# Kernel tuning notes

Measured on AMD Instinct MI355X. Metric: run time of the kernel, lower is better.

## Reference

```python
import jax, jax.numpy as jnp
import numpy as np

EPS = 1e-5
FT_DEPTH = 5
FT_SMOOTH = 1e-5


def _conv(x, w):
    # x: [B,H,W,Cin], w: [kh,kw,Cin,Cout], SAME padding, stride 1
    return jax.lax.conv_general_dilated(x, w, (1, 1), 'SAME',
                                         dimension_numbers=('NHWC', 'HWIO', 'NHWC'))


def _bn(x, g, b, m, v):
    # inference-mode batch norm over last axis
    return (x - m) * jax.lax.rsqrt(v + EPS) * g + b


def _ftanimoto(p, l, axis):
    # Fractal Tanimoto similarity with keepdims, averaged over FT_DEPTH scales.
    tpl = jnp.sum(p * l, axis=axis, keepdims=True)
    tpp = jnp.sum(p * p, axis=axis, keepdims=True)
    tll = jnp.sum(l * l, axis=axis, keepdims=True)
    num = tpl + FT_SMOOTH
    denum = jnp.zeros_like(tpl)
    for d in range(FT_DEPTH):
        a = 2.0 ** d
        b = -(2.0 * a - 1.0)
        denum = denum + 1.0 / (a * (tpp + tll) + b * tpl + FT_SMOOTH)
    return num * denum * (1.0 / FT_DEPTH)


def setup_inputs() -> dict:
    key = jax.random.key(0)
    ks = jax.random.split(key, 24)
    B, H, W, C = 8, 128, 128, 96
    d = {}
    d['x1'] = jax.random.normal(ks[0], (B, H, W, C), jnp.float32)
    d['x2'] = jax.random.normal(ks[1], (B, H, W, C), jnp.float32)
    d['x3'] = jax.random.normal(ks[2], (B, H, W, C), jnp.float32)
    d['wq'] = jax.random.normal(ks[3], (3, 3, C, C), jnp.float32) * 0.05
    d['gq'] = jax.random.uniform(ks[4], (C,), jnp.float32)
    d['bq'] = jax.random.normal(ks[5], (C,), jnp.float32) * 0.1
    d['mq'] = jax.random.normal(ks[6], (C,), jnp.float32) * 0.1
    d['vq'] = jax.random.uniform(ks[7], (C,), jnp.float32) + 0.5
    d['wk'] = jax.random.normal(ks[8], (3, 3, C, C), jnp.float32) * 0.05
    d['gk'] = jax.random.uniform(ks[9], (C,), jnp.float32)
    d['bk'] = jax.random.normal(ks[10], (C,), jnp.float32) * 0.1
    d['mk'] = jax.random.normal(ks[11], (C,), jnp.float32) * 0.1
    d['vk'] = jax.random.uniform(ks[12], (C,), jnp.float32) + 0.5
    d['wv'] = jax.random.normal(ks[13], (3, 3, C, C), jnp.float32) * 0.05
    d['gv'] = jax.random.uniform(ks[14], (C,), jnp.float32)
    d['bv'] = jax.random.normal(ks[15], (C,), jnp.float32) * 0.1
    d['mv'] = jax.random.normal(ks[16], (C,), jnp.float32) * 0.1
    d['vv'] = jax.random.uniform(ks[17], (C,), jnp.float32) + 0.5
    d['gn'] = jax.random.uniform(ks[18], (C,), jnp.float32)
    d['bnb'] = jax.random.normal(ks[19], (C,), jnp.float32) * 0.1
    d['mn'] = jax.random.normal(ks[20], (C,), jnp.float32) * 0.1
    d['vn'] = jax.random.uniform(ks[21], (C,), jnp.float32) + 0.5
    return d


def reference(x1, x2, x3, wq, gq, bq, mq, vq, wk, gk, bk, mk, vk,
              wv, gv, bv, mv, vv, gn, bnb, mn, vn):
    q = jax.nn.sigmoid(_bn(_conv(x1, wq), gq, bq, mq, vq))   # [B,H,W,C]
    k = jax.nn.sigmoid(_bn(_conv(x2, wk), gk, bk, mk, vk))
    v = jax.nn.sigmoid(_bn(_conv(x3, wv), gv, bv, mv, vv))
    att_spat = _ftanimoto(q, k, axis=-1)        # [B,H,W,1] spatial attention
    att_chan = _ftanimoto(q, k, axis=(1, 2))    # [B,1,1,C] channel attention
    v_cspat = 0.5 * (att_chan * v + att_spat * v)
    return _bn(v_cspat, gn, bnb, mn, vn)
```

## Files before the change

### kernel.cpp

```cpp
#include <hip/hip_runtime.h>
#include <hip/hip_bf16.h>
#include <math.h>

#define BB 8
#define HH 128
#define WW 128
#define CC 96
#define NPIX (BB*HH*WW)
#define EPSF 1e-5f
#define FT_SMOOTH_F 1e-5f
#define ROWB 8320
#define WELEM 82944

typedef short short8 __attribute__((ext_vector_type(8)));
typedef float f32x4 __attribute__((ext_vector_type(4)));

__device__ __forceinline__ float ftanimoto(float tpl, float tpp, float tll) {
    float num = tpl + FT_SMOOTH_F;
    float denum = 0.0f;
    float a = 1.0f;
#pragma unroll
    for (int d = 0; d < 5; ++d) {
        float bco = -(2.0f * a - 1.0f);
        denum += 1.0f / (a * (tpp + tll) + bco * tpl + FT_SMOOTH_F);
        a *= 2.0f;
    }
    return num * denum * 0.2f;
}

__device__ __forceinline__ unsigned short f2bf(float f) {
    __hip_bfloat16 h = __float2bfloat16(f);
    return *(unsigned short*)&h;
}

__device__ __forceinline__ float bf2f(unsigned short u) {
    return __uint_as_float((unsigned int)u << 16);
}

__global__ __launch_bounds__(256) void cast_wT2(
    const float* __restrict__ wq, const float* __restrict__ wk,
    const float* __restrict__ wv, unsigned short* __restrict__ wT2)
{
    const int tid = blockIdx.x * 256 + threadIdx.x;
    if (tid >= 3 * WELEM) return;
    const int cid = tid / WELEM;
    const int o = tid - cid * WELEM;
    const int j = o & 7;
    const int rest = o >> 3;
    const int lq = rest & 63;
    const int lrow = lq >> 2, qq = lq & 3;
    const int tile = rest >> 6;
    const int nt = tile % 6;
    const int tcc = tile / 6;
    const int cc = tcc % 3, tap = tcc / 3;
    const int ci = cc * 32 + qq * 8 + j;
    const int co = nt * 16 + lrow;
    const float* w = (cid == 0) ? wq : (cid == 1) ? wk : wv;
    wT2[tid] = f2bf(w[(size_t)(tap * CC + ci) * CC + co]);
}

__global__ __launch_bounds__(256, 3) void conv_all(
    const float* __restrict__ x1, const float* __restrict__ x2,
    const float* __restrict__ x3, const unsigned short* __restrict__ wT2,
    const float* __restrict__ gq, const float* __restrict__ bq,
    const float* __restrict__ mq, const float* __restrict__ vq,
    const float* __restrict__ gk, const float* __restrict__ bk,
    const float* __restrict__ mk, const float* __restrict__ vk,
    const float* __restrict__ gv, const float* __restrict__ bv,
    const float* __restrict__ mv, const float* __restrict__ vv,
    unsigned short* __restrict__ qb, unsigned short* __restrict__ kb,
    unsigned short* __restrict__ vb)
{
    __shared__ __align__(16) char smem[4 * ROWB];
    const int tid = threadIdx.x;
    const int wv = tid >> 6;
    const int L  = tid & 63;
    const int cid = blockIdx.x >> 9;
    const int blk = blockIdx.x & 511;
    const int b  = blk >> 6;
    const int h0 = (blk & 63) << 1;
    const int hrow = h0 + (wv >> 1);
    const int wwbase = (wv & 1) << 6;
    const int lrow = L & 15;
    const int qq = L >> 4;

    const float* xsrc = (cid == 0) ? x1 : (cid == 1) ? x2 : x3;
    const unsigned short* wT2p = wT2 + (size_t)cid * WELEM;

    const int hst = h0 - 1 + wv;
    const bool stv = (hst >= 0) && (hst < HH);
    const float* xrow = xsrc + (size_t)(b * HH + (stv ? hst : 0)) * WW * CC;
    char* myrow = smem + wv * ROWB;

    f32x4 acc[4][6];
#pragma unroll
    for (int mt = 0; mt < 4; ++mt)
#pragma unroll
        for (int nt = 0; nt < 6; ++nt) acc[mt][nt] = (f32x4){0.f, 0.f, 0.f, 0.f};

    for (int cc = 0; cc < 3; ++cc) {
        __syncthreads();
        if (stv) {
#pragma unroll
            for (int it = 0; it < 9; ++it) {
                const int idx = it * 64 + L;
                if (idx < 520) {
                    const int p = idx >> 2;
                    const int c = idx & 3;
                    const int w = p - 1;
                    short8 o = (short8){0,0,0,0,0,0,0,0};
                    if (w >= 0 && w < WW) {
                        const float* src = xrow + (size_t)w * CC + cc * 32 + c * 8;
                        const float4 a0 = *(const float4*)src;
                        const float4 a1 = *(const float4*)(src + 4);
                        o[0] = (short)f2bf(a0.x); o[1] = (short)f2bf(a0.y);
                        o[2] = (short)f2bf(a0.z); o[3] = (short)f2bf(a0.w);
                        o[4] = (short)f2bf(a1.x); o[5] = (short)f2bf(a1.y);
                        o[6] = (short)f2bf(a1.z); o[7] = (short)f2bf(a1.w);
                    }
                    const int slot = c ^ ((p ^ (p >> 2)) & 3);
                    *(short8*)(myrow + p * 64 + slot * 16) = o;
                }
            }
        }
        __syncthreads();
#pragma unroll
        for (int dy = -1; dy <= 1; ++dy) {
            const int hh = hrow + dy;
            if (hh < 0 || hh >= HH) continue;
            const char* ldsrow = smem + (dy + 1 + (wv >> 1)) * ROWB;
#pragma unroll
            for (int dx = -1; dx <= 1; ++dx) {
                const int tap = (dy + 1) * 3 + (dx + 1);
                const unsigned short* bsrc = wT2p + (size_t)(tap * 3 + cc) * 6 * 512;
                short8 bf[6];
#pragma unroll
                for (int nt = 0; nt < 6; ++nt)
                    bf[nt] = *(const short8*)(bsrc + nt * 512 + (lrow * 4 + qq) * 8);
                short8 af[4];
#pragma unroll
                for (int mt = 0; mt < 4; ++mt) {
                    const int p = wwbase + mt * 16 + lrow + dx + 1;
                    const int slot = qq ^ ((p ^ (p >> 2)) & 3);
                    af[mt] = *(const short8*)(ldsrow + p * 64 + slot * 16);
                }
#pragma unroll
                for (int nt = 0; nt < 6; ++nt)
#pragma unroll
                    for (int mt = 0; mt < 4; ++mt)
                        acc[mt][nt] = __builtin_amdgcn_mfma_f32_16x16x32_bf16(
                            af[mt], bf[nt], acc[mt][nt], 0, 0, 0);
            }
        }
    }

    const float* g  = (cid == 0) ? gq : (cid == 1) ? gk : gv;
    const float* bt = (cid == 0) ? bq : (cid == 1) ? bk : bv;
    const float* mu = (cid == 0) ? mq : (cid == 1) ? mk : mv;
    const float* var = (cid == 0) ? vq : (cid == 1) ? vk : vv;
    unsigned short* outp = (cid == 0) ? qb : (cid == 1) ? kb : vb;

#pragma unroll
    for (int nt = 0; nt < 6; ++nt) {
        const int co = nt * 16 + lrow;
        const float scl = g[co] * rsqrtf(var[co] + EPSF);
        const float sft = bt[co] - mu[co] * scl;
#pragma unroll
        for (int mt = 0; mt < 4; ++mt) {
#pragma unroll
            for (int r = 0; r < 4; ++r) {
                const int row = (wv << 6) + (mt << 4) + (qq << 2) + r;
                const int h = h0 + (row >> 7);
                const int w = row & 127;
                const size_t pix = (size_t)(b * HH + h) * WW + w;
                const float t = acc[mt][nt][r] * scl + sft;
                outp[pix * CC + co] = f2bf(1.0f / (1.0f + expf(-t)));
            }
        }
    }
}

__global__ __launch_bounds__(256) void spatial_att(
    const unsigned short* __restrict__ qb, const unsigned short* __restrict__ kb,
    float* __restrict__ atts)
{
    const int gid = blockIdx.x * 256 + threadIdx.x;
    const int pix = gid >> 6;
    const int lane = threadIdx.x & 63;
    float tpl = 0.f, tpp = 0.f, tll = 0.f;
    if (lane < 48) {
        const unsigned int qu = ((const unsigned int*)qb)[(size_t)pix * 48 + lane];
        const unsigned int ku = ((const unsigned int*)kb)[(size_t)pix * 48 + lane];
        const float q0 = __uint_as_float(qu << 16);
        const float q1 = __uint_as_float(qu & 0xffff0000u);
        const float k0 = __uint_as_float(ku << 16);
        const float k1 = __uint_as_float(ku & 0xffff0000u);
        tpl = q0 * k0 + q1 * k1;
        tpp = q0 * q0 + q1 * q1;
        tll = k0 * k0 + k1 * k1;
    }
#pragma unroll
    for (int off = 32; off > 0; off >>= 1) {
        tpl += __shfl_xor(tpl, off);
        tpp += __shfl_xor(tpp, off);
        tll += __shfl_xor(tll, off);
    }
    if (lane == 0) atts[pix] = ftanimoto(tpl, tpp, tll);
}

__global__ __launch_bounds__(192) void chan_partial(
    const unsigned short* __restrict__ qb, const unsigned short* __restrict__ kb,
    float* __restrict__ part)
{
    __shared__ float red[16][12][24];
    const int t = threadIdx.x;
    const int g = t / 12;
    const int c8 = t - g * 12;
    const int b = blockIdx.x >> 6;
    const int slab = blockIdx.x & 63;
    const size_t p0 = (size_t)b * HH * WW + (size_t)slab * 256;

    float s_tpl[8], s_tpp[8], s_tll[8];
#pragma unroll
    for (int j = 0; j < 8; ++j) { s_tpl[j] = 0.f; s_tpp[j] = 0.f; s_tll[j] = 0.f; }

    for (int i = 0; i < 16; ++i) {
        const size_t pe = (p0 + g + i * 16) * CC + c8 * 8;
        const short8 qv = *(const short8*)(qb + pe);
        const short8 kv = *(const short8*)(kb + pe);
#pragma unroll
        for (int j = 0; j < 8; ++j) {
            const float qf = bf2f((unsigned short)qv[j]);
            const float kf = bf2f((unsigned short)kv[j]);
            s_tpl[j] = fmaf(qf, kf, s_tpl[j]);
            s_tpp[j] = fmaf(qf, qf, s_tpp[j]);
            s_tll[j] = fmaf(kf, kf, s_tll[j]);
        }
    }
#pragma unroll
    for (int j = 0; j < 8; ++j) {
        red[g][c8][0 * 8 + j] = s_tpl[j];
        red[g][c8][1 * 8 + j] = s_tpp[j];
        red[g][c8][2 * 8 + j] = s_tll[j];
    }
    __syncthreads();
    if (t < CC) {
        const int cg = t >> 3, cj = t & 7;
        float tpl = 0.f, tpp = 0.f, tll = 0.f;
        for (int gg = 0; gg < 16; ++gg) {
            tpl += red[gg][cg][0 * 8 + cj];
            tpp += red[gg][cg][1 * 8 + cj];
            tll += red[gg][cg][2 * 8 + cj];
        }
        const size_t idx = ((size_t)blockIdx.x * CC + t) * 3;
        part[idx + 0] = tpl;
        part[idx + 1] = tpp;
        part[idx + 2] = tll;
    }
}

__global__ __launch_bounds__(128) void chan_final(
    const float* __restrict__ part, float* __restrict__ attc)
{
    const int b = blockIdx.x;
    const int c = threadIdx.x;
    if (c >= CC) return;
    float tpl = 0.f, tpp = 0.f, tll = 0.f;
    for (int s = 0; s < 64; ++s) {
        const size_t idx = (((size_t)(b * 64 + s)) * CC + c) * 3;
        tpl += part[idx + 0];
        tpp += part[idx + 1];
        tll += part[idx + 2];
    }
    attc[b * CC + c] = ftanimoto(tpl, tpp, tll);
}

__global__ __launch_bounds__(256) void final_combine(
    const unsigned short* __restrict__ vb, const float* __restrict__ atts,
    const float* __restrict__ attc,
    const float* __restrict__ gn, const float* __restrict__ bnb,
    const float* __restrict__ mn, const float* __restrict__ vn,
    float* __restrict__ out)
{
    const int tid = blockIdx.x * 256 + threadIdx.x;
    const int c8 = tid % 12;
    const int pix = tid / 12;
    const int b = pix >> 14;
    const short8 v = *(const short8*)(vb + (size_t)pix * CC + c8 * 8);
    const float as = atts[pix];
    float r[8];
#pragma unroll
    for (int j = 0; j < 8; ++j) {
        const int co = c8 * 8 + j;
        const float nscl = gn[co] * rsqrtf(vn[co] + EPSF);
        const float nsft = bnb[co] - mn[co] * nscl;
        const float att = 0.5f * (attc[b * CC + co] + as);
        r[j] = att * bf2f((unsigned short)v[j]) * nscl + nsft;
    }
    float* dst = out + (size_t)pix * CC + c8 * 8;
    *(float4*)dst = make_float4(r[0], r[1], r[2], r[3]);
    *(float4*)(dst + 4) = make_float4(r[4], r[5], r[6], r[7]);
}

extern "C" void kernel_launch(void* const* d_in, const int* in_sizes, int n_in,
                              void* d_out, int out_size, void* d_ws, size_t ws_size,
                              hipStream_t stream)
{
    const float* x1 = (const float*)d_in[0];
    const float* x2 = (const float*)d_in[1];
    const float* x3 = (const float*)d_in[2];
    const float* wq = (const float*)d_in[3];
    const float* gq = (const float*)d_in[4];
    const float* bq = (const float*)d_in[5];
    const float* mq = (const float*)d_in[6];
    const float* vq = (const float*)d_in[7];
    const float* wk = (const float*)d_in[8];
    const float* gk = (const float*)d_in[9];
    const float* bk = (const float*)d_in[10];
    const float* mk = (const float*)d_in[11];
    const float* vk = (const float*)d_in[12];
    const float* wvw = (const float*)d_in[13];
    const float* gv = (const float*)d_in[14];
    const float* bv = (const float*)d_in[15];
    const float* mv = (const float*)d_in[16];
    const float* vv = (const float*)d_in[17];
    const float* gn = (const float*)d_in[18];
    const float* bnb = (const float*)d_in[19];
    const float* mn = (const float*)d_in[20];
    const float* vn = (const float*)d_in[21];

    unsigned short* wT2 = (unsigned short*)d_ws;
    unsigned short* vb = wT2 + (size_t)3 * WELEM;
    float* atts = (float*)(vb + (size_t)NPIX * CC);
    float* part = atts + NPIX;
    float* attc = part + (size_t)512 * CC * 3;

    unsigned short* qb = (unsigned short*)d_out;
    unsigned short* kb = qb + (size_t)NPIX * CC;

    cast_wT2<<<(3 * WELEM + 255) / 256, 256, 0, stream>>>(wq, wk, wvw, wT2);
    conv_all<<<1536, 256, 0, stream>>>(x1, x2, x3, wT2,
                                       gq, bq, mq, vq, gk, bk, mk, vk,
                                       gv, bv, mv, vv, qb, kb, vb);
    spatial_att<<<NPIX / 4, 256, 0, stream>>>(qb, kb, atts);
    chan_partial<<<BB * 64, 192, 0, stream>>>(qb, kb, part);
    chan_final<<<BB, 128, 0, stream>>>(part, attc);
    final_combine<<<NPIX * 12 / 256, 256, 0, stream>>>(vb, atts, attc,
                                                       gn, bnb, mn, vn,
                                                       (float*)d_out);
}
```

Before: 366.5 us.

## Prefetch conv input into registers and fuse spatial and channel attention reductions

The conv kernel now loads the next channel chunk of input rows into registers while MFMA runs on the current chunk, so global load latency overlaps with compute. The occupancy hint drops from 3 to 2 blocks to make room for the extra registers. The separate spatial-attention and channel-partial kernels are merged into one pass that reads q and k once and produces both per-pixel and per-channel sums via shared memory. The channel final reduction becomes a wave-per-channel shuffle reduction. This adds register pressure and shared memory use in exchange for less global traffic and fewer launches.

```diff
diff --git a/kernel.cpp b/kernel.cpp
--- a/kernel.cpp
+++ b/kernel.cpp
@@ -59,7 +59,7 @@
     wT2[tid] = f2bf(w[(size_t)(tap * CC + ci) * CC + co]);
 }
 
-__global__ __launch_bounds__(256, 3) void conv_all(
+__global__ __launch_bounds__(256, 2) void conv_all(
     const float* __restrict__ x1, const float* __restrict__ x2,
     const float* __restrict__ x3, const unsigned short* __restrict__ wT2,
     const float* __restrict__ gq, const float* __restrict__ bq,
@@ -73,24 +73,24 @@
 {
     __shared__ __align__(16) char smem[4 * ROWB];
     const int tid = threadIdx.x;
-    const int wv = tid >> 6;
+    const int wvi = tid >> 6;
     const int L  = tid & 63;
     const int cid = blockIdx.x >> 9;
     const int blk = blockIdx.x & 511;
     const int b  = blk >> 6;
     const int h0 = (blk & 63) << 1;
-    const int hrow = h0 + (wv >> 1);
-    const int wwbase = (wv & 1) << 6;
+    const int hrow = h0 + (wvi >> 1);
+    const int wwbase = (wvi & 1) << 6;
     const int lrow = L & 15;
     const int qq = L >> 4;
 
     const float* xsrc = (cid == 0) ? x1 : (cid == 1) ? x2 : x3;
     const unsigned short* wT2p = wT2 + (size_t)cid * WELEM;
 
-    const int hst = h0 - 1 + wv;
+    const int hst = h0 - 1 + wvi;
     const bool stv = (hst >= 0) && (hst < HH);
     const float* xrow = xsrc + (size_t)(b * HH + (stv ? hst : 0)) * WW * CC;
-    char* myrow = smem + wv * ROWB;
+    char* myrow = smem + wvi * ROWB;
 
     f32x4 acc[4][6];
 #pragma unroll
@@ -98,61 +98,85 @@
 #pragma unroll
         for (int nt = 0; nt < 6; ++nt) acc[mt][nt] = (f32x4){0.f, 0.f, 0.f, 0.f};
 
-    for (int cc = 0; cc < 3; ++cc) {
-        __syncthreads();
-        if (stv) {
-#pragma unroll
-            for (int it = 0; it < 9; ++it) {
-                const int idx = it * 64 + L;
-                if (idx < 520) {
-                    const int p = idx >> 2;
-                    const int c = idx & 3;
-                    const int w = p - 1;
-                    short8 o = (short8){0,0,0,0,0,0,0,0};
-                    if (w >= 0 && w < WW) {
-                        const float* src = xrow + (size_t)w * CC + cc * 32 + c * 8;
-                        const float4 a0 = *(const float4*)src;
-                        const float4 a1 = *(const float4*)(src + 4);
-                        o[0] = (short)f2bf(a0.x); o[1] = (short)f2bf(a0.y);
-                        o[2] = (short)f2bf(a0.z); o[3] = (short)f2bf(a0.w);
-                        o[4] = (short)f2bf(a1.x); o[5] = (short)f2bf(a1.y);
-                        o[6] = (short)f2bf(a1.z); o[7] = (short)f2bf(a1.w);
-                    }
-                    const int slot = c ^ ((p ^ (p >> 2)) & 3);
-                    *(short8*)(myrow + p * 64 + slot * 16) = o;
-                }
-            }
-        }
-        __syncthreads();
-#pragma unroll
-        for (int dy = -1; dy <= 1; ++dy) {
-            const int hh = hrow + dy;
-            if (hh < 0 || hh >= HH) continue;
-            const char* ldsrow = smem + (dy + 1 + (wv >> 1)) * ROWB;
-#pragma unroll
-            for (int dx = -1; dx <= 1; ++dx) {
-                const int tap = (dy + 1) * 3 + (dx + 1);
-                const unsigned short* bsrc = wT2p + (size_t)(tap * 3 + cc) * 6 * 512;
-                short8 bf[6];
-#pragma unroll
-                for (int nt = 0; nt < 6; ++nt)
-                    bf[nt] = *(const short8*)(bsrc + nt * 512 + (lrow * 4 + qq) * 8);
-                short8 af[4];
-#pragma unroll
-                for (int mt = 0; mt < 4; ++mt) {
-                    const int p = wwbase + mt * 16 + lrow + dx + 1;
-                    const int slot = qq ^ ((p ^ (p >> 2)) & 3);
-                    af[mt] = *(const short8*)(ldsrow + p * 64 + slot * 16);
-                }
-#pragma unroll
-                for (int nt = 0; nt < 6; ++nt)
-#pragma unroll
-                    for (int mt = 0; mt < 4; ++mt)
-                        acc[mt][nt] = __builtin_amdgcn_mfma_f32_16x16x32_bf16(
-                            af[mt], bf[nt], acc[mt][nt], 0, 0, 0);
-            }
-        }
-    }
+    float4 pre[9][2];
+
+#define PREF(ccv) do { if (stv) { _Pragma("unroll") \
+    for (int it = 0; it < 9; ++it) { \
+        const int idx = it * 64 + L; \
+        if (idx < 520) { \
+            const int p = idx >> 2; \
+            const int c = idx & 3; \
+            const int w = p - 1; \
+            if (w >= 0 && w < WW) { \
+                const float* src = xrow + (size_t)w * CC + (ccv) * 32 + c * 8; \
+                pre[it][0] = *(const float4*)src; \
+                pre[it][1] = *(const float4*)(src + 4); \
+            } } } } } while (0)
+
+#define WST() do { if (stv) { _Pragma("unroll") \
+    for (int it = 0; it < 9; ++it) { \
+        const int idx = it * 64 + L; \
+        if (idx < 520) { \
+            const int p = idx >> 2; \
+            const int c = idx & 3; \
+            const int w = p - 1; \
+            short8 o = (short8){0,0,0,0,0,0,0,0}; \
+            if (w >= 0 && w < WW) { \
+                o[0] = (short)f2bf(pre[it][0].x); o[1] = (short)f2bf(pre[it][0].y); \
+                o[2] = (short)f2bf(pre[it][0].z); o[3] = (short)f2bf(pre[it][0].w); \
+                o[4] = (short)f2bf(pre[it][1].x); o[5] = (short)f2bf(pre[it][1].y); \
+                o[6] = (short)f2bf(pre[it][1].z); o[7] = (short)f2bf(pre[it][1].w); \
+            } \
+            const int slot = c ^ ((p ^ (p >> 2)) & 3); \
+            *(short8*)(myrow + p * 64 + slot * 16) = o; \
+        } } } } while (0)
+
+#define COMPUTE(ccv) do { _Pragma("unroll") \
+    for (int dy = -1; dy <= 1; ++dy) { \
+        const int hh = hrow + dy; \
+        if (hh < 0 || hh >= HH) continue; \
+        const char* ldsrow = smem + (dy + 1 + (wvi >> 1)) * ROWB; \
+        _Pragma("unroll") \
+        for (int dx = -1; dx <= 1; ++dx) { \
+            const int tap = (dy + 1) * 3 + (dx + 1); \
+            const unsigned short* bsrc = wT2p + (size_t)(tap * 3 + (ccv)) * 6 * 512; \
+            short8 bfr[6]; \
+            _Pragma("unroll") \
+            for (int nt = 0; nt < 6; ++nt) \
+                bfr[nt] = *(const short8*)(bsrc + nt * 512 + (lrow * 4 + qq) * 8); \
+            short8 afr[4]; \
+            _Pragma("unroll") \
+            for (int mt = 0; mt < 4; ++mt) { \
+                const int p = wwbase + mt * 16 + lrow + dx + 1; \
+                const int slot = qq ^ ((p ^ (p >> 2)) & 3); \
+                afr[mt] = *(const short8*)(ldsrow + p * 64 + slot * 16); \
+            } \
+            _Pragma("unroll") \
+            for (int nt = 0; nt < 6; ++nt) \
+                _Pragma("unroll") \
+                for (int mt = 0; mt < 4; ++mt) \
+                    acc[mt][nt] = __builtin_amdgcn_mfma_f32_16x16x32_bf16( \
+                        afr[mt], bfr[nt], acc[mt][nt], 0, 0, 0); \
+        } } } while (0)
+
+    PREF(0);
+    WST();
+    __syncthreads();
+    PREF(1);
+    COMPUTE(0);
+    __syncthreads();
+    WST();
+    __syncthreads();
+    PREF(2);
+    COMPUTE(1);
+    __syncthreads();
+    WST();
+    __syncthreads();
+    COMPUTE(2);
+
+#undef PREF
+#undef WST
+#undef COMPUTE
 
     const float* g  = (cid == 0) ? gq : (cid == 1) ? gk : gv;
     const float* bt = (cid == 0) ? bq : (cid == 1) ? bk : bv;
@@ -169,7 +193,7 @@
         for (int mt = 0; mt < 4; ++mt) {
 #pragma unroll
             for (int r = 0; r < 4; ++r) {
-                const int row = (wv << 6) + (mt << 4) + (qq << 2) + r;
+                const int row = (wvi << 6) + (mt << 4) + (qq << 2) + r;
                 const int h = h0 + (row >> 7);
                 const int w = row & 127;
                 const size_t pix = (size_t)(b * HH + h) * WW + w;
@@ -180,54 +204,28 @@
     }
 }
 
-__global__ __launch_bounds__(256) void spatial_att(
+__global__ __launch_bounds__(192) void qk_att(
     const unsigned short* __restrict__ qb, const unsigned short* __restrict__ kb,
-    float* __restrict__ atts)
-{
-    const int gid = blockIdx.x * 256 + threadIdx.x;
-    const int pix = gid >> 6;
-    const int lane = threadIdx.x & 63;
-    float tpl = 0.f, tpp = 0.f, tll = 0.f;
-    if (lane < 48) {
-        const unsigned int qu = ((const unsigned int*)qb)[(size_t)pix * 48 + lane];
-        const unsigned int ku = ((const unsigned int*)kb)[(size_t)pix * 48 + lane];
-        const float q0 = __uint_as_float(qu << 16);
-        const float q1 = __uint_as_float(qu & 0xffff0000u);
-        const float k0 = __uint_as_float(ku << 16);
-        const float k1 = __uint_as_float(ku & 0xffff0000u);
-        tpl = q0 * k0 + q1 * k1;
-        tpp = q0 * q0 + q1 * q1;
-        tll = k0 * k0 + k1 * k1;
-    }
-#pragma unroll
-    for (int off = 32; off > 0; off >>= 1) {
-        tpl += __shfl_xor(tpl, off);
-        tpp += __shfl_xor(tpp, off);
-        tll += __shfl_xor(tll, off);
-    }
-    if (lane == 0) atts[pix] = ftanimoto(tpl, tpp, tll);
-}
-
-__global__ __launch_bounds__(192) void chan_partial(
-    const unsigned short* __restrict__ qb, const unsigned short* __restrict__ kb,
-    float* __restrict__ part)
-{
+    float* __restrict__ atts, float* __restrict__ part)
+{
+    __shared__ float pxr[256][37];
     __shared__ float red[16][12][24];
     const int t = threadIdx.x;
     const int g = t / 12;
     const int c8 = t - g * 12;
-    const int b = blockIdx.x >> 6;
-    const int slab = blockIdx.x & 63;
-    const size_t p0 = (size_t)b * HH * WW + (size_t)slab * 256;
+    const size_t p0 = (size_t)blockIdx.x * 256;
 
     float s_tpl[8], s_tpp[8], s_tll[8];
 #pragma unroll
     for (int j = 0; j < 8; ++j) { s_tpl[j] = 0.f; s_tpp[j] = 0.f; s_tll[j] = 0.f; }
 
+#pragma unroll
     for (int i = 0; i < 16; ++i) {
-        const size_t pe = (p0 + g + i * 16) * CC + c8 * 8;
+        const int px = g + i * 16;
+        const size_t pe = (p0 + px) * CC + c8 * 8;
         const short8 qv = *(const short8*)(qb + pe);
         const short8 kv = *(const short8*)(kb + pe);
+        float ptpl = 0.f, ptpp = 0.f, ptll = 0.f;
 #pragma unroll
         for (int j = 0; j < 8; ++j) {
             const float qf = bf2f((unsigned short)qv[j]);
@@ -235,22 +233,40 @@
             s_tpl[j] = fmaf(qf, kf, s_tpl[j]);
             s_tpp[j] = fmaf(qf, qf, s_tpp[j]);
             s_tll[j] = fmaf(kf, kf, s_tll[j]);
+            ptpl = fmaf(qf, kf, ptpl);
+            ptpp = fmaf(qf, qf, ptpp);
+            ptll = fmaf(kf, kf, ptll);
         }
+        pxr[px][c8 * 3 + 0] = ptpl;
+        pxr[px][c8 * 3 + 1] = ptpp;
+        pxr[px][c8 * 3 + 2] = ptll;
     }
 #pragma unroll
     for (int j = 0; j < 8; ++j) {
-        red[g][c8][0 * 8 + j] = s_tpl[j];
-        red[g][c8][1 * 8 + j] = s_tpp[j];
-        red[g][c8][2 * 8 + j] = s_tll[j];
-    }
-    __syncthreads();
+        red[g][c8][j]      = s_tpl[j];
+        red[g][c8][8 + j]  = s_tpp[j];
+        red[g][c8][16 + j] = s_tll[j];
+    }
+    __syncthreads();
+
+    for (int px = t; px < 256; px += 192) {
+        float tpl = 0.f, tpp = 0.f, tll = 0.f;
+#pragma unroll
+        for (int c = 0; c < 12; ++c) {
+            tpl += pxr[px][c * 3 + 0];
+            tpp += pxr[px][c * 3 + 1];
+            tll += pxr[px][c * 3 + 2];
+        }
+        atts[p0 + px] = ftanimoto(tpl, tpp, tll);
+    }
+
     if (t < CC) {
         const int cg = t >> 3, cj = t & 7;
         float tpl = 0.f, tpp = 0.f, tll = 0.f;
         for (int gg = 0; gg < 16; ++gg) {
-            tpl += red[gg][cg][0 * 8 + cj];
-            tpp += red[gg][cg][1 * 8 + cj];
-            tll += red[gg][cg][2 * 8 + cj];
+            tpl += red[gg][cg][cj];
+            tpp += red[gg][cg][8 + cj];
+            tll += red[gg][cg][16 + cj];
         }
         const size_t idx = ((size_t)blockIdx.x * CC + t) * 3;
         part[idx + 0] = tpl;
@@ -259,20 +275,24 @@
     }
 }
 
-__global__ __launch_bounds__(128) void chan_final(
+__global__ __launch_bounds__(256) void chan_final2(
     const float* __restrict__ part, float* __restrict__ attc)
 {
-    const int b = blockIdx.x;
-    const int c = threadIdx.x;
-    if (c >= CC) return;
-    float tpl = 0.f, tpp = 0.f, tll = 0.f;
-    for (int s = 0; s < 64; ++s) {
-        const size_t idx = (((size_t)(b * 64 + s)) * CC + c) * 3;
-        tpl += part[idx + 0];
-        tpp += part[idx + 1];
-        tll += part[idx + 2];
-    }
-    attc[b * CC + c] = ftanimoto(tpl, tpp, tll);
+    const int wid = blockIdx.x * 4 + (threadIdx.x >> 6);
+    const int lane = threadIdx.x & 63;
+    const int b = wid / CC;
+    const int c = wid - b * CC;
+    const size_t idx = (((size_t)b * 64 + lane) * CC + c) * 3;
+    float tpl = part[idx + 0];
+    float tpp = part[idx + 1];
+    float tll = part[idx + 2];
+#pragma unroll
+    for (int off = 32; off > 0; off >>= 1) {
+        tpl += __shfl_xor(tpl, off);
+        tpp += __shfl_xor(tpp, off);
+        tll += __shfl_xor(tll, off);
+    }
+    if (lane == 0) attc[b * CC + c] = ftanimoto(tpl, tpp, tll);
 }
 
 __global__ __launch_bounds__(256) void final_combine(
@@ -342,9 +362,8 @@
     conv_all<<<1536, 256, 0, stream>>>(x1, x2, x3, wT2,
                                        gq, bq, mq, vq, gk, bk, mk, vk,
                                        gv, bv, mv, vv, qb, kb, vb);
-    spatial_att<<<NPIX / 4, 256, 0, stream>>>(qb, kb, atts);
-    chan_partial<<<BB * 64, 192, 0, stream>>>(qb, kb, part);
-    chan_final<<<BB, 128, 0, stream>>>(part, attc);
+    qk_att<<<NPIX / 256, 192, 0, stream>>>(qb, kb, atts, part);
+    chan_final2<<<192, 256, 0, stream>>>(part, attc);
     final_combine<<<NPIX * 12 / 256, 256, 0, stream>>>(vb, atts, attc,
                                                        gn, bnb, mn, vn,
                                                        (float*)d_out);
```

New measurement: 336.7 us. 1.09x faster.

## Fuse spatial and channel attention reductions into one pass over q/k

Applied to the files above, without the earlier changes.

Merges the spatial-attention kernel and the channel partial-reduction kernel into a single kernel that reads q and k once. Each block handles 128 pixels, reduces per-pixel sums through shared memory, and emits channel partials. The channel final reduction becomes a wave-per-channel shuffle reduction over 128 partials. The conv epilogue sigmoid also switches to exp2/rcp intrinsics. This removes a full extra read of the bf16 q/k tensors, at the cost of twice as many partials, more shared memory and less precise sigmoid math.

```diff
diff --git a/kernel.cpp b/kernel.cpp
--- a/kernel.cpp
+++ b/kernel.cpp
@@ -174,60 +174,35 @@
                 const int w = row & 127;
                 const size_t pix = (size_t)(b * HH + h) * WW + w;
                 const float t = acc[mt][nt][r] * scl + sft;
-                outp[pix * CC + co] = f2bf(1.0f / (1.0f + expf(-t)));
+                const float e = __builtin_amdgcn_exp2f(t * -1.442695041f);
+                outp[pix * CC + co] = f2bf(__builtin_amdgcn_rcpf(1.0f + e));
             }
         }
     }
 }
 
-__global__ __launch_bounds__(256) void spatial_att(
+__global__ __launch_bounds__(192) void qk_att(
     const unsigned short* __restrict__ qb, const unsigned short* __restrict__ kb,
-    float* __restrict__ atts)
-{
-    const int gid = blockIdx.x * 256 + threadIdx.x;
-    const int pix = gid >> 6;
-    const int lane = threadIdx.x & 63;
-    float tpl = 0.f, tpp = 0.f, tll = 0.f;
-    if (lane < 48) {
-        const unsigned int qu = ((const unsigned int*)qb)[(size_t)pix * 48 + lane];
-        const unsigned int ku = ((const unsigned int*)kb)[(size_t)pix * 48 + lane];
-        const float q0 = __uint_as_float(qu << 16);
-        const float q1 = __uint_as_float(qu & 0xffff0000u);
-        const float k0 = __uint_as_float(ku << 16);
-        const float k1 = __uint_as_float(ku & 0xffff0000u);
-        tpl = q0 * k0 + q1 * k1;
-        tpp = q0 * q0 + q1 * q1;
-        tll = k0 * k0 + k1 * k1;
-    }
-#pragma unroll
-    for (int off = 32; off > 0; off >>= 1) {
-        tpl += __shfl_xor(tpl, off);
-        tpp += __shfl_xor(tpp, off);
-        tll += __shfl_xor(tll, off);
-    }
-    if (lane == 0) atts[pix] = ftanimoto(tpl, tpp, tll);
-}
-
-__global__ __launch_bounds__(192) void chan_partial(
-    const unsigned short* __restrict__ qb, const unsigned short* __restrict__ kb,
-    float* __restrict__ part)
-{
+    float* __restrict__ atts, float* __restrict__ part)
+{
+    __shared__ float pxr[128][37];
     __shared__ float red[16][12][24];
     const int t = threadIdx.x;
     const int g = t / 12;
     const int c8 = t - g * 12;
-    const int b = blockIdx.x >> 6;
-    const int slab = blockIdx.x & 63;
-    const size_t p0 = (size_t)b * HH * WW + (size_t)slab * 256;
+    const size_t p0 = (size_t)blockIdx.x * 128;
 
     float s_tpl[8], s_tpp[8], s_tll[8];
 #pragma unroll
     for (int j = 0; j < 8; ++j) { s_tpl[j] = 0.f; s_tpp[j] = 0.f; s_tll[j] = 0.f; }
 
-    for (int i = 0; i < 16; ++i) {
-        const size_t pe = (p0 + g + i * 16) * CC + c8 * 8;
+#pragma unroll
+    for (int i = 0; i < 8; ++i) {
+        const int px = g + i * 16;
+        const size_t pe = (p0 + px) * CC + c8 * 8;
         const short8 qv = *(const short8*)(qb + pe);
         const short8 kv = *(const short8*)(kb + pe);
+        float ptpl = 0.f, ptpp = 0.f, ptll = 0.f;
 #pragma unroll
         for (int j = 0; j < 8; ++j) {
             const float qf = bf2f((unsigned short)qv[j]);
@@ -235,22 +210,40 @@
             s_tpl[j] = fmaf(qf, kf, s_tpl[j]);
             s_tpp[j] = fmaf(qf, qf, s_tpp[j]);
             s_tll[j] = fmaf(kf, kf, s_tll[j]);
-        }
+            ptpl = fmaf(qf, kf, ptpl);
+            ptpp = fmaf(qf, qf, ptpp);
+            ptll = fmaf(kf, kf, ptll);
+        }
+        pxr[px][c8 * 3 + 0] = ptpl;
+        pxr[px][c8 * 3 + 1] = ptpp;
+        pxr[px][c8 * 3 + 2] = ptll;
     }
 #pragma unroll
     for (int j = 0; j < 8; ++j) {
-        red[g][c8][0 * 8 + j] = s_tpl[j];
-        red[g][c8][1 * 8 + j] = s_tpp[j];
-        red[g][c8][2 * 8 + j] = s_tll[j];
+        red[g][c8][j]      = s_tpl[j];
+        red[g][c8][8 + j]  = s_tpp[j];
+        red[g][c8][16 + j] = s_tll[j];
     }
     __syncthreads();
+
+    if (t < 128) {
+        float tpl = 0.f, tpp = 0.f, tll = 0.f;
+#pragma unroll
+        for (int c = 0; c < 12; ++c) {
+            tpl += pxr[t][c * 3 + 0];
+            tpp += pxr[t][c * 3 + 1];
+            tll += pxr[t][c * 3 + 2];
+        }
+        atts[p0 + t] = ftanimoto(tpl, tpp, tll);
+    }
+
     if (t < CC) {
         const int cg = t >> 3, cj = t & 7;
         float tpl = 0.f, tpp = 0.f, tll = 0.f;
         for (int gg = 0; gg < 16; ++gg) {
-            tpl += red[gg][cg][0 * 8 + cj];
-            tpp += red[gg][cg][1 * 8 + cj];
-            tll += red[gg][cg][2 * 8 + cj];
+            tpl += red[gg][cg][cj];
+            tpp += red[gg][cg][8 + cj];
+            tll += red[gg][cg][16 + cj];
         }
         const size_t idx = ((size_t)blockIdx.x * CC + t) * 3;
         part[idx + 0] = tpl;
@@ -259,20 +252,25 @@
     }
 }
 
-__global__ __launch_bounds__(128) void chan_final(
+__global__ __launch_bounds__(256) void chan_final2(
     const float* __restrict__ part, float* __restrict__ attc)
 {
-    const int b = blockIdx.x;
-    const int c = threadIdx.x;
-    if (c >= CC) return;
-    float tpl = 0.f, tpp = 0.f, tll = 0.f;
-    for (int s = 0; s < 64; ++s) {
-        const size_t idx = (((size_t)(b * 64 + s)) * CC + c) * 3;
-        tpl += part[idx + 0];
-        tpp += part[idx + 1];
-        tll += part[idx + 2];
-    }
-    attc[b * CC + c] = ftanimoto(tpl, tpp, tll);
+    const int wid = blockIdx.x * 4 + (threadIdx.x >> 6);
+    const int lane = threadIdx.x & 63;
+    const int b = wid / CC;
+    const int c = wid - b * CC;
+    const size_t base = (((size_t)b * 128 + lane) * CC + c) * 3;
+    const size_t off = (size_t)64 * CC * 3;
+    float tpl = part[base + 0] + part[base + off + 0];
+    float tpp = part[base + 1] + part[base + off + 1];
+    float tll = part[base + 2] + part[base + off + 2];
+#pragma unroll
+    for (int off2 = 32; off2 > 0; off2 >>= 1) {
+        tpl += __shfl_xor(tpl, off2);
+        tpp += __shfl_xor(tpp, off2);
+        tll += __shfl_xor(tll, off2);
+    }
+    if (lane == 0) attc[b * CC + c] = ftanimoto(tpl, tpp, tll);
 }
 
 __global__ __launch_bounds__(256) void final_combine(
@@ -333,7 +331,7 @@
     unsigned short* vb = wT2 + (size_t)3 * WELEM;
     float* atts = (float*)(vb + (size_t)NPIX * CC);
     float* part = atts + NPIX;
-    float* attc = part + (size_t)512 * CC * 3;
+    float* attc = part + (size_t)1024 * CC * 3;
 
     unsigned short* qb = (unsigned short*)d_out;
     unsigned short* kb = qb + (size_t)NPIX * CC;
@@ -342,9 +340,8 @@
     conv_all<<<1536, 256, 0, stream>>>(x1, x2, x3, wT2,
                                        gq, bq, mq, vq, gk, bk, mk, vk,
                                        gv, bv, mv, vv, qb, kb, vb);
-    spatial_att<<<NPIX / 4, 256, 0, stream>>>(qb, kb, atts);
-    chan_partial<<<BB * 64, 192, 0, stream>>>(qb, kb, part);
-    chan_final<<<BB, 128, 0, stream>>>(part, attc);
+    qk_att<<<NPIX / 128, 192, 0, stream>>>(qb, kb, atts, part);
+    chan_final2<<<192, 256, 0, stream>>>(part, attc);
     final_combine<<<NPIX * 12 / 256, 256, 0, stream>>>(vb, atts, attc,
                                                        gn, bnb, mn, vn,
                                                        (float*)d_out);
```

Result: faster. 326.0 us (-11.1%).
